# Optimization experiments

Measured on AMD Instinct MI355X. Metric: run time of the kernel, lower is better.

## Reference

```python
import jax, jax.numpy as jnp
import numpy as np


def squash(v, axis=-1):
    # scale = |v|^2 / (1+|v|^2) / |v|  (exactly as in the source)
    s2 = jnp.sum(jnp.square(v), axis=axis, keepdims=True)
    scale = s2 / (1.0 + s2) / jnp.sqrt(s2)
    return scale * v


def setup_inputs() -> dict:
    key = jax.random.key(0)
    k1, k2 = jax.random.split(key)
    B, I, P = 64, 2048, 16   # batch, input_num_capsule, input_dim_vector
    J, D = 32, 32            # num_capsule, dim_vector
    inputs = jax.random.normal(k1, (B, I, P), dtype=jnp.float32)
    W = jax.random.normal(k2, (I, J, P, D), dtype=jnp.float32) * 0.1
    bias = jnp.zeros((1, I, J, 1, 1), dtype=jnp.float32)
    return {"inputs": inputs, "W": W, "bias": bias}


def reference(inputs, W, bias):
    # inputs_hat[b,i,j,d] = inputs[b,i,:] @ W[i,j,:,:]
    # (replaces the tf.scan over batch of per-capsule batch_dot)
    inputs_hat = jnp.einsum('bip,ijpd->bijd', inputs, W)

    # In the source while_loop, c = softmax(self.bias, dim=2) is computed from the
    # ORIGINAL bias every iteration (loop-carried b is never read), so all
    # num_routing iterations yield the identical output; compute it once.
    c = jax.nn.softmax(bias[:, :, :, 0, 0], axis=2)          # [1, I, J]
    s = jnp.einsum('bijd,xij->bjd', inputs_hat, c)            # sum over input capsules
    outputs = squash(s, axis=-1)                              # [B, J, D]
    return outputs
```

## Files before the change

kernel.cpp:

```cpp
#include <hip/hip_runtime.h>
#include <hip/hip_bf16.h>
#include <math.h>

#define I_CAP 2048
#define P_DIM 16
#define J_CAP 32
#define D_DIM 32
#define B_SZ  64
#define KCN   32
#define IPB   (I_CAP / KCN)
#define NWAVE 8
#define IPW   (IPB / NWAVE)

typedef __attribute__((ext_vector_type(8)))  short short8_t;
typedef __attribute__((ext_vector_type(16))) float f32x16;

__device__ __forceinline__ short f2bf(float f) {
    __hip_bfloat16 h = __float2bfloat16(f);
    return __builtin_bit_cast(short, h);
}

__global__ __launch_bounds__(512, 2) void caps_main_k(const float* __restrict__ inputs,
                                                      const float* __restrict__ W,
                                                      const float* __restrict__ bias,
                                                      float* __restrict__ partial) {
    __shared__ float red[NWAVE * 2048];
    __shared__ float c_lds[IPB][4];
    const int t  = threadIdx.x;
    const int l  = t & 63;
    const int wv = t >> 6;

    const int orig = blockIdx.x;
    const int wgid = (orig & 7) * 32 + (orig >> 3);
    const int kc = wgid >> 3;
    const int jq = wgid & 7;
    const int j0 = jq * 4;

    const int g  = l >> 5;
    const int dn = l & 31;

    const int i0blk = kc * IPB;
    const int i0    = i0blk + wv * IPW;

    {
        const int jj = t & 31;
        const int ib = t >> 5;
        const int jr = jj - j0;
#pragma unroll
        for (int pass = 0; pass < 4; ++pass) {
            const int ii = pass * 16 + ib;
            float x = bias[(i0blk + ii) * J_CAP + jj];
            float m = x;
#pragma unroll
            for (int k = 16; k >= 1; k >>= 1) m = fmaxf(m, __shfl_xor(m, k));
            float e = expf(x - m);
            float s = e;
#pragma unroll
            for (int k = 16; k >= 1; k >>= 1) s += __shfl_xor(s, k);
            if ((unsigned)jr < 4u) c_lds[ii][jr] = e / s;
        }
    }
    __syncthreads();

    const float* wlane  = W + (((size_t)(i0 * J_CAP + j0)) << 9) + g * 256 + dn;
    const float* alane0 = inputs + ((size_t)dn << 15) + (size_t)i0 * 16 + g * 8;
    const float* alane1 = alane0 + ((size_t)32 << 15);

    f32x16 acc[4][2];
#pragma unroll
    for (int jj = 0; jj < 4; ++jj) { acc[jj][0] = (f32x16){}; acc[jj][1] = (f32x16){}; }

#pragma unroll 2
    for (int r = 0; r < IPW; ++r) {
        float wb[4][8];
#pragma unroll
        for (int jj = 0; jj < 4; ++jj)
#pragma unroll
            for (int e = 0; e < 8; ++e)
                wb[jj][e] = wlane[(size_t)r * 16384 + jj * 512 + e * 32];

        float4 a0 = *(const float4*)(alane0 + r * 16);
        float4 a1 = *(const float4*)(alane0 + r * 16 + 4);
        float4 a2 = *(const float4*)(alane1 + r * 16);
        float4 a3 = *(const float4*)(alane1 + r * 16 + 4);

        short8_t af0, af1;
        af0[0] = f2bf(a0.x); af0[1] = f2bf(a0.y); af0[2] = f2bf(a0.z); af0[3] = f2bf(a0.w);
        af0[4] = f2bf(a1.x); af0[5] = f2bf(a1.y); af0[6] = f2bf(a1.z); af0[7] = f2bf(a1.w);
        af1[0] = f2bf(a2.x); af1[1] = f2bf(a2.y); af1[2] = f2bf(a2.z); af1[3] = f2bf(a2.w);
        af1[4] = f2bf(a3.x); af1[5] = f2bf(a3.y); af1[6] = f2bf(a3.z); af1[7] = f2bf(a3.w);

#pragma unroll
        for (int jj = 0; jj < 4; ++jj) {
            const float cj = c_lds[wv * IPW + r][jj];
            short8_t bf;
#pragma unroll
            for (int e = 0; e < 8; ++e) bf[e] = f2bf(wb[jj][e] * cj);
            acc[jj][0] = __builtin_amdgcn_mfma_f32_32x32x16_bf16(af0, bf, acc[jj][0], 0, 0, 0);
            acc[jj][1] = __builtin_amdgcn_mfma_f32_32x32x16_bf16(af1, bf, acc[jj][1], 0, 0, 0);
        }
    }

#pragma unroll
    for (int jj = 0; jj < 4; ++jj) {
        __syncthreads();
        {
            float* rw = red + wv * 2048;
#pragma unroll
            for (int reg = 0; reg < 16; ++reg) {
                const int b0 = (reg & 3) + 8 * (reg >> 2) + 4 * g;
                rw[b0 * 32 + dn]        = acc[jj][0][reg];
                rw[(b0 + 32) * 32 + dn] = acc[jj][1][reg];
            }
        }
        __syncthreads();
        {
            const int o = t * 4;
            float4 v = {0.f, 0.f, 0.f, 0.f};
#pragma unroll
            for (int w8 = 0; w8 < NWAVE; ++w8) {
                float4 p = *(const float4*)(red + w8 * 2048 + o);
                v.x += p.x; v.y += p.y; v.z += p.z; v.w += p.w;
            }
            *(float4*)(partial + (size_t)(kc * J_CAP + j0 + jj) * 2048 + o) = v;
        }
    }
}

__global__ __launch_bounds__(256) void caps_reduce_squash_k(const float* __restrict__ partial,
                                                            float* __restrict__ out) {
    const int tid2 = blockIdx.x * 256 + threadIdx.x;
    const int row  = tid2 >> 4;
    const int sub  = tid2 & 15;
    const int d4   = sub >> 1;
    const int half = sub & 1;
    const int j = row >> 6, b = row & 63;

    const float* src = partial + ((size_t)(half * 16) * J_CAP + j) * 2048 + b * 32 + d4 * 4;
    float4 v = {0.f, 0.f, 0.f, 0.f};
#pragma unroll
    for (int kc = 0; kc < 16; ++kc) {
        float4 p = *(const float4*)(src + (size_t)kc * J_CAP * 2048);
        v.x += p.x; v.y += p.y; v.z += p.z; v.w += p.w;
    }
    v.x += __shfl_xor(v.x, 1); v.y += __shfl_xor(v.y, 1);
    v.z += __shfl_xor(v.z, 1); v.w += __shfl_xor(v.w, 1);

    float sq = v.x * v.x + v.y * v.y + v.z * v.z + v.w * v.w;
#pragma unroll
    for (int m = 2; m <= 8; m <<= 1) sq += __shfl_xor(sq, m);
    float scale = sq / (1.0f + sq) / sqrtf(sq);
    if (half == 0) {
        float4 o = {v.x * scale, v.y * scale, v.z * scale, v.w * scale};
        *(float4*)(out + (size_t)b * (J_CAP * D_DIM) + j * D_DIM + d4 * 4) = o;
    }
}

extern "C" void kernel_launch(void* const* d_in, const int* in_sizes, int n_in,
                              void* d_out, int out_size, void* d_ws, size_t ws_size,
                              hipStream_t stream) {
    const float* inputs = (const float*)d_in[0];
    const float* W      = (const float*)d_in[1];
    const float* bias   = (const float*)d_in[2];
    float* out = (float*)d_out;

    float* partial = (float*)d_ws;

    caps_main_k<<<dim3(KCN * 8), dim3(512), 0, stream>>>(inputs, W, bias, partial);
    caps_reduce_squash_k<<<dim3(128), dim3(256), 0, stream>>>(partial, out);
}
```

Before: 35.37 us.

## Double-buffer W via async global-to-LDS loads and prefetch inputs in registers

```diff
diff --git a/kernel.cpp b/kernel.cpp
--- a/kernel.cpp
+++ b/kernel.cpp
@@ -20,12 +20,17 @@
     return __builtin_bit_cast(short, h);
 }
 
+#define GLOAD_LDS16(gp, lp)                                                     \
+    __builtin_amdgcn_global_load_lds(                                           \
+        (const __attribute__((address_space(1))) void*)(gp),                    \
+        (__attribute__((address_space(3))) void*)(lp), 16, 0, 0)
+
 __global__ __launch_bounds__(512, 2) void caps_main_k(const float* __restrict__ inputs,
                                                       const float* __restrict__ W,
                                                       const float* __restrict__ bias,
                                                       float* __restrict__ partial) {
-    __shared__ float red[NWAVE * 2048];
-    __shared__ float c_lds[IPB][4];
+    __shared__ float lds[33024];
+    float* c_lds = lds + 32768;
     const int t  = threadIdx.x;
     const int l  = t & 63;
     const int wv = t >> 6;
@@ -42,6 +47,21 @@
     const int i0blk = kc * IPB;
     const int i0    = i0blk + wv * IPW;
 
+    float* wbuf = lds + wv * 4096;
+
+    const float* wsrc   = W + (((size_t)(i0 * J_CAP + j0)) << 9) + l * 4;
+    const float* alane0 = inputs + ((size_t)dn << 15) + (size_t)i0 * 16 + g * 8;
+    const float* alane1 = alane0 + ((size_t)32 << 15);
+
+    float4 aP[2][4];
+#pragma unroll
+    for (int n = 0; n < 8; ++n)
+        GLOAD_LDS16(wsrc + n * 256, wbuf + n * 256);
+    aP[0][0] = *(const float4*)(alane0);
+    aP[0][1] = *(const float4*)(alane0 + 4);
+    aP[0][2] = *(const float4*)(alane1);
+    aP[0][3] = *(const float4*)(alane1 + 4);
+
     {
         const int jj = t & 31;
         const int ib = t >> 5;
@@ -57,45 +77,52 @@
             float s = e;
 #pragma unroll
             for (int k = 16; k >= 1; k >>= 1) s += __shfl_xor(s, k);
-            if ((unsigned)jr < 4u) c_lds[ii][jr] = e / s;
+            if ((unsigned)jr < 4u) c_lds[ii * 4 + jr] = e / s;
         }
     }
     __syncthreads();
-
-    const float* wlane  = W + (((size_t)(i0 * J_CAP + j0)) << 9) + g * 256 + dn;
-    const float* alane0 = inputs + ((size_t)dn << 15) + (size_t)i0 * 16 + g * 8;
-    const float* alane1 = alane0 + ((size_t)32 << 15);
 
     f32x16 acc[4][2];
 #pragma unroll
     for (int jj = 0; jj < 4; ++jj) { acc[jj][0] = (f32x16){}; acc[jj][1] = (f32x16){}; }
 
-#pragma unroll 2
+#pragma unroll
     for (int r = 0; r < IPW; ++r) {
-        float wb[4][8];
+        const int pb = r & 1;
+        if (r + 1 < IPW) {
+            const float* ws = wsrc + (size_t)(r + 1) * 16384;
+            float* wd = wbuf + (pb ^ 1) * 2048;
 #pragma unroll
-        for (int jj = 0; jj < 4; ++jj)
-#pragma unroll
-            for (int e = 0; e < 8; ++e)
-                wb[jj][e] = wlane[(size_t)r * 16384 + jj * 512 + e * 32];
+            for (int n = 0; n < 8; ++n)
+                GLOAD_LDS16(ws + n * 256, wd + n * 256);
+            aP[pb ^ 1][0] = *(const float4*)(alane0 + (r + 1) * 16);
+            aP[pb ^ 1][1] = *(const float4*)(alane0 + (r + 1) * 16 + 4);
+            aP[pb ^ 1][2] = *(const float4*)(alane1 + (r + 1) * 16);
+            aP[pb ^ 1][3] = *(const float4*)(alane1 + (r + 1) * 16 + 4);
+        }
+        __builtin_amdgcn_sched_barrier(0);
+        if (r + 1 < IPW) asm volatile("s_waitcnt vmcnt(12)" ::: "memory");
+        else             asm volatile("s_waitcnt vmcnt(0)" ::: "memory");
+        __builtin_amdgcn_sched_barrier(0);
 
-        float4 a0 = *(const float4*)(alane0 + r * 16);
-        float4 a1 = *(const float4*)(alane0 + r * 16 + 4);
-        float4 a2 = *(const float4*)(alane1 + r * 16);
-        float4 a3 = *(const float4*)(alane1 + r * 16 + 4);
-
+        const float* wb = wbuf + pb * 2048;
         short8_t af0, af1;
-        af0[0] = f2bf(a0.x); af0[1] = f2bf(a0.y); af0[2] = f2bf(a0.z); af0[3] = f2bf(a0.w);
-        af0[4] = f2bf(a1.x); af0[5] = f2bf(a1.y); af0[6] = f2bf(a1.z); af0[7] = f2bf(a1.w);
-        af1[0] = f2bf(a2.x); af1[1] = f2bf(a2.y); af1[2] = f2bf(a2.z); af1[3] = f2bf(a2.w);
-        af1[4] = f2bf(a3.x); af1[5] = f2bf(a3.y); af1[6] = f2bf(a3.z); af1[7] = f2bf(a3.w);
+        af0[0] = f2bf(aP[pb][0].x); af0[1] = f2bf(aP[pb][0].y);
+        af0[2] = f2bf(aP[pb][0].z); af0[3] = f2bf(aP[pb][0].w);
+        af0[4] = f2bf(aP[pb][1].x); af0[5] = f2bf(aP[pb][1].y);
+        af0[6] = f2bf(aP[pb][1].z); af0[7] = f2bf(aP[pb][1].w);
+        af1[0] = f2bf(aP[pb][2].x); af1[1] = f2bf(aP[pb][2].y);
+        af1[2] = f2bf(aP[pb][2].z); af1[3] = f2bf(aP[pb][2].w);
+        af1[4] = f2bf(aP[pb][3].x); af1[5] = f2bf(aP[pb][3].y);
+        af1[6] = f2bf(aP[pb][3].z); af1[7] = f2bf(aP[pb][3].w);
 
 #pragma unroll
         for (int jj = 0; jj < 4; ++jj) {
-            const float cj = c_lds[wv * IPW + r][jj];
+            const float cj = c_lds[(wv * IPW + r) * 4 + jj];
             short8_t bf;
 #pragma unroll
-            for (int e = 0; e < 8; ++e) bf[e] = f2bf(wb[jj][e] * cj);
+            for (int e = 0; e < 8; ++e)
+                bf[e] = f2bf(wb[jj * 512 + (g * 8 + e) * 32 + dn] * cj);
             acc[jj][0] = __builtin_amdgcn_mfma_f32_32x32x16_bf16(af0, bf, acc[jj][0], 0, 0, 0);
             acc[jj][1] = __builtin_amdgcn_mfma_f32_32x32x16_bf16(af1, bf, acc[jj][1], 0, 0, 0);
         }
@@ -105,7 +132,7 @@
     for (int jj = 0; jj < 4; ++jj) {
         __syncthreads();
         {
-            float* rw = red + wv * 2048;
+            float* rw = lds + wv * 4096;
 #pragma unroll
             for (int reg = 0; reg < 16; ++reg) {
                 const int b0 = (reg & 3) + 8 * (reg >> 2) + 4 * g;
@@ -119,7 +146,7 @@
             float4 v = {0.f, 0.f, 0.f, 0.f};
 #pragma unroll
             for (int w8 = 0; w8 < NWAVE; ++w8) {
-                float4 p = *(const float4*)(red + w8 * 2048 + o);
+                float4 p = *(const float4*)(lds + w8 * 4096 + o);
                 v.x += p.x; v.y += p.y; v.z += p.z; v.w += p.w;
             }
             *(float4*)(partial + (size_t)(kc * J_CAP + j0 + jj) * 2048 + o) = v;
```

After: 35.31 us. Within noise of the previous version (-0.1%).

## Split batch across workgroups to double grid size and raise occupancy

Applied to the files above, without the earlier changes.

```diff
diff --git a/kernel.cpp b/kernel.cpp
--- a/kernel.cpp
+++ b/kernel.cpp
@@ -20,20 +20,21 @@
     return __builtin_bit_cast(short, h);
 }
 
-__global__ __launch_bounds__(512, 2) void caps_main_k(const float* __restrict__ inputs,
+__global__ __launch_bounds__(512, 4) void caps_main_k(const float* __restrict__ inputs,
                                                       const float* __restrict__ W,
                                                       const float* __restrict__ bias,
                                                       float* __restrict__ partial) {
-    __shared__ float red[NWAVE * 2048];
+    __shared__ float red[NWAVE * 1024];
     __shared__ float c_lds[IPB][4];
     const int t  = threadIdx.x;
     const int l  = t & 63;
     const int wv = t >> 6;
 
     const int orig = blockIdx.x;
-    const int wgid = (orig & 7) * 32 + (orig >> 3);
-    const int kc = wgid >> 3;
-    const int jq = wgid & 7;
+    const int wgid = (orig & 7) * 64 + (orig >> 3);
+    const int kc = wgid >> 4;
+    const int jq = (wgid >> 1) & 7;
+    const int bh = wgid & 1;
     const int j0 = jq * 4;
 
     const int g  = l >> 5;
@@ -62,42 +63,38 @@
     }
     __syncthreads();
 
-    const float* wlane  = W + (((size_t)(i0 * J_CAP + j0)) << 9) + g * 256 + dn;
-    const float* alane0 = inputs + ((size_t)dn << 15) + (size_t)i0 * 16 + g * 8;
-    const float* alane1 = alane0 + ((size_t)32 << 15);
+    const float* wlane = W + (((size_t)(i0 * J_CAP + j0)) << 9) + g * 256 + dn;
+    const float* asrc  = inputs + (size_t)(bh * 32 + dn) * 32768 + (size_t)i0 * 16 + g * 8;
 
-    f32x16 acc[4][2];
+    f32x16 acc[4];
 #pragma unroll
-    for (int jj = 0; jj < 4; ++jj) { acc[jj][0] = (f32x16){}; acc[jj][1] = (f32x16){}; }
+    for (int jj = 0; jj < 4; ++jj) acc[jj] = (f32x16){};
 
 #pragma unroll 2
     for (int r = 0; r < IPW; ++r) {
-        float wb[4][8];
-#pragma unroll
-        for (int jj = 0; jj < 4; ++jj)
-#pragma unroll
-            for (int e = 0; e < 8; ++e)
-                wb[jj][e] = wlane[(size_t)r * 16384 + jj * 512 + e * 32];
-
-        float4 a0 = *(const float4*)(alane0 + r * 16);
-        float4 a1 = *(const float4*)(alane0 + r * 16 + 4);
-        float4 a2 = *(const float4*)(alane1 + r * 16);
-        float4 a3 = *(const float4*)(alane1 + r * 16 + 4);
-
-        short8_t af0, af1;
-        af0[0] = f2bf(a0.x); af0[1] = f2bf(a0.y); af0[2] = f2bf(a0.z); af0[3] = f2bf(a0.w);
-        af0[4] = f2bf(a1.x); af0[5] = f2bf(a1.y); af0[6] = f2bf(a1.z); af0[7] = f2bf(a1.w);
-        af1[0] = f2bf(a2.x); af1[1] = f2bf(a2.y); af1[2] = f2bf(a2.z); af1[3] = f2bf(a2.w);
-        af1[4] = f2bf(a3.x); af1[5] = f2bf(a3.y); af1[6] = f2bf(a3.z); af1[7] = f2bf(a3.w);
+        float4 a0 = *(const float4*)(asrc + r * 16);
+        float4 a1 = *(const float4*)(asrc + r * 16 + 4);
+        short8_t af;
+        af[0] = f2bf(a0.x); af[1] = f2bf(a0.y); af[2] = f2bf(a0.z); af[3] = f2bf(a0.w);
+        af[4] = f2bf(a1.x); af[5] = f2bf(a1.y); af[6] = f2bf(a1.z); af[7] = f2bf(a1.w);
 
 #pragma unroll
-        for (int jj = 0; jj < 4; ++jj) {
-            const float cj = c_lds[wv * IPW + r][jj];
-            short8_t bf;
+        for (int jh = 0; jh < 2; ++jh) {
+            float wb[2][8];
 #pragma unroll
-            for (int e = 0; e < 8; ++e) bf[e] = f2bf(wb[jj][e] * cj);
-            acc[jj][0] = __builtin_amdgcn_mfma_f32_32x32x16_bf16(af0, bf, acc[jj][0], 0, 0, 0);
-            acc[jj][1] = __builtin_amdgcn_mfma_f32_32x32x16_bf16(af1, bf, acc[jj][1], 0, 0, 0);
+            for (int q = 0; q < 2; ++q)
+#pragma unroll
+                for (int e = 0; e < 8; ++e)
+                    wb[q][e] = wlane[(size_t)r * 16384 + (jh * 2 + q) * 512 + e * 32];
+#pragma unroll
+            for (int q = 0; q < 2; ++q) {
+                const int jj = jh * 2 + q;
+                const float cj = c_lds[wv * IPW + r][jj];
+                short8_t bf;
+#pragma unroll
+                for (int e = 0; e < 8; ++e) bf[e] = f2bf(wb[q][e] * cj);
+                acc[jj] = __builtin_amdgcn_mfma_f32_32x32x16_bf16(af, bf, acc[jj], 0, 0, 0);
+            }
         }
     }
 
@@ -105,24 +102,23 @@
     for (int jj = 0; jj < 4; ++jj) {
         __syncthreads();
         {
-            float* rw = red + wv * 2048;
+            float* rw = red + wv * 1024;
 #pragma unroll
             for (int reg = 0; reg < 16; ++reg) {
                 const int b0 = (reg & 3) + 8 * (reg >> 2) + 4 * g;
-                rw[b0 * 32 + dn]        = acc[jj][0][reg];
-                rw[(b0 + 32) * 32 + dn] = acc[jj][1][reg];
+                rw[b0 * 32 + dn] = acc[jj][reg];
             }
         }
         __syncthreads();
         {
-            const int o = t * 4;
-            float4 v = {0.f, 0.f, 0.f, 0.f};
+            const int o = t * 2;
+            float2 v = {0.f, 0.f};
 #pragma unroll
             for (int w8 = 0; w8 < NWAVE; ++w8) {
-                float4 p = *(const float4*)(red + w8 * 2048 + o);
-                v.x += p.x; v.y += p.y; v.z += p.z; v.w += p.w;
+                float2 p = *(const float2*)(red + w8 * 1024 + o);
+                v.x += p.x; v.y += p.y;
             }
-            *(float4*)(partial + (size_t)(kc * J_CAP + j0 + jj) * 2048 + o) = v;
+            *(float2*)(partial + (size_t)(kc * J_CAP + j0 + jj) * 2048 + bh * 1024 + o) = v;
         }
     }
 }
@@ -166,6 +162,6 @@
 
     float* partial = (float*)d_ws;
 
-    caps_main_k<<<dim3(KCN * 8), dim3(512), 0, stream>>>(inputs, W, bias, partial);
+    caps_main_k<<<dim3(KCN * 8 * 2), dim3(512), 0, stream>>>(inputs, W, bias, partial);
     caps_reduce_squash_k<<<dim3(128), dim3(256), 0, stream>>>(partial, out);
 }
```

Result: slower. 36.26 us (+2.5%).
